# Optimization experiments

Hardware: AMD Instinct MI355X
Metric: run time of the kernel (lower is better)

## Reference

```python
import jax, jax.numpy as jnp
import numpy as np

B, S, D, V = 2, 256, 512, 32000
W_WIN, GAMMA = 20, 2.0
MEM_LEN, NUM_MEM, K_SIM, K_CONT = 16, 256, 8, 4


def _modularity(sim, bnd):
    deg = sim.sum(1)
    tot = deg.sum()
    com = jnp.cumsum(bnd).astype(jnp.int32)
    exp = deg[:, None] * deg[None, :] / (tot + 1e-10)
    mask = (com[:, None] == com[None, :]).astype(sim.dtype)
    return ((sim - exp) * mask).sum() / (tot + 1e-10)


def _conductance(sim, bnd):
    n = sim.shape[0]
    deg = sim.sum(1)
    tot = deg.sum()
    com = jnp.cumsum(bnd).astype(jnp.int32)
    oh = jax.nn.one_hot(com, n + 1, dtype=sim.dtype)  # [N, N+1] fixed class count (empty communities contribute 0)
    vol = oh.T @ deg
    inter = oh.T @ sim @ oh
    inter = inter * (1.0 - jnp.eye(n + 1, dtype=sim.dtype))
    cuts = inter.sum(1)
    minv = jnp.minimum(vol, tot - vol)
    cond = cuts / (minv + 1e-10)
    # torch averages over num_communities = max(com)+1
    return cond.sum() / (com[-1].astype(sim.dtype) + 1.0)


def _forward(query, key, value, attention_mask, target_tokens, brain_w,
             storage_w1, storage_b1, storage_w2, storage_b2, sim_w, sim_b,
             memory_keys, memory_values, memory_lengths, memory_timestamps):
    # --- surprise: per-token NLL of target under brain logits ---
    logits = jnp.einsum('bsd,vd->bsv', query, brain_w)
    logp = jax.nn.log_softmax(logits, axis=-1)
    surprise = -jnp.take_along_axis(logp, target_tokens[..., None], axis=-1)[..., 0]  # [B,S]
    # --- dynamic threshold over sliding windows (unbiased std, as torch) ---
    widx = jnp.arange(S - W_WIN + 1)[:, None] + jnp.arange(W_WIN)[None, :]
    win = surprise[:, widx]  # [B, S-W+1, W]
    thr = win.mean(-1) + GAMMA * jnp.std(win, axis=-1, ddof=1)
    thr = jnp.concatenate([jnp.repeat(thr[:, :1], W_WIN - 1, axis=1), thr], axis=1)
    boundaries = (surprise > thr).astype(query.dtype)  # [B,S]
    # --- refine boundaries via modularity / conductance on token similarity graph ---
    sims = jnp.einsum('bnd,bmd->bnm', query, query)
    curQ = jax.vmap(_modularity)(sims, boundaries)
    curC = jax.vmap(_conductance)(sims, boundaries)
    b_idx = jnp.repeat(jnp.arange(B), S)
    t_idx = jnp.tile(jnp.arange(S), B)

    def cand(b, t):  # evaluate removing boundary at (b,t)
        tb = boundaries[b].at[t].set(0.0)
        return _modularity(sims[b], tb), _conductance(sims[b], tb)

    newQ, newC = jax.vmap(cand)(b_idx, t_idx)
    impr = ((newQ > curQ[b_idx]) | (newC < curC[b_idx])).reshape(B, S)
    refined = jnp.where((boundaries > 0) & impr, 0.0, boundaries)
    # --- event segmentation: labels via cumsum; position-in-event via cummax of segment starts ---
    labels = jnp.cumsum(refined, axis=1).astype(jnp.int32)  # [B,S] in [0,S]
    t_r = jnp.arange(S)
    changed = jnp.concatenate([jnp.ones((B, 1), bool), labels[:, 1:] != labels[:, :-1]], axis=1)
    start = jax.lax.cummax(jnp.where(changed, t_r[None, :], 0), axis=1)
    pos = t_r[None, :] - start  # [B,S] position within event
    bflat = jnp.repeat(jnp.arange(B), S)
    lflat = labels.reshape(-1)
    pflat = pos.reshape(-1)  # tokens with pos >= MEM_LEN are truncated (OOB -> dropped)
    events = jnp.zeros((B, S + 1, MEM_LEN, D), query.dtype)
    events = events.at[bflat, lflat, pflat].add(query.reshape(-1, D), mode='drop')
    counts = jnp.zeros((B, S + 1), jnp.int32).at[bflat, lflat].add(1)
    # --- pack non-empty events into circular memory bank (memory_index = 0, timestamp = 0) ---
    flat_ev = events.reshape(B * (S + 1), MEM_LEN, D)
    flat_ct = counts.reshape(-1)
    nonempty = flat_ct > 0
    rank = jnp.cumsum(nonempty) - 1
    slot = jnp.where(nonempty, rank % NUM_MEM, NUM_MEM)  # OOB slot -> dropped
    mem_keys = memory_keys.at[slot].set(flat_ev[:, 0, :], mode='drop')
    mem_vals = memory_values.at[slot].set(flat_ev, mode='drop')
    mem_lens = memory_lengths.at[slot].set(jnp.minimum(flat_ct, MEM_LEN).astype(memory_lengths.dtype), mode='drop')
    mem_ts = memory_timestamps.at[slot].set(jnp.zeros(slot.shape, memory_timestamps.dtype), mode='drop')
    # --- retrieval: kNN over memory keys with projected mean query ---
    qm = (jnp.einsum('bsd,ed->bse', query, sim_w) + sim_b).mean(1)  # [B,D]
    scores = qm @ mem_keys.T  # [B, NUM_MEM]
    valid = mem_lens > 0
    scores = jnp.where(valid[None, :], scores, -1e9)
    _, top_i = jax.lax.top_k(scores, K_SIM)
    sim_buf = mem_vals[top_i].reshape(B, K_SIM * MEM_LEN, D)
    rec = jnp.where(valid, jnp.arange(NUM_MEM), -1)  # contiguity = most recently written slots
    _, cont_i = jax.lax.top_k(rec, K_CONT)
    cont_buf = jnp.broadcast_to(mem_vals[cont_i].reshape(1, K_CONT * MEM_LEN, D), (B, K_CONT * MEM_LEN, D))
    storage = lambda x: jax.nn.relu(x @ storage_w1.T + storage_b1) @ storage_w2.T + storage_b2
    context = jnp.concatenate([storage(sim_buf), storage(cont_buf), key], axis=1)  # [B, 192+S, D]
    mem_total = (K_SIM + K_CONT) * MEM_LEN
    ext_mask = jnp.concatenate([jnp.ones((B, mem_total), attention_mask.dtype), attention_mask], axis=1)
    return query, context, context, ext_mask


def setup_inputs():
    rng = jax.random.key(0)
    ks = jax.random.split(rng, 10)
    sc = 0.02
    return {
        'query': jax.random.normal(ks[0], (B, S, D), jnp.float32),
        'key': jax.random.normal(ks[1], (B, S, D), jnp.float32),
        'value': jax.random.normal(ks[2], (B, S, D), jnp.float32),
        'attention_mask': jnp.ones((B, S), jnp.float32),
        'target_tokens': jax.random.randint(ks[3], (B, S), 0, V),
        'brain_w': jax.random.normal(ks[4], (V, D), jnp.float32) * sc,
        'storage_w1': jax.random.normal(ks[5], (D, D), jnp.float32) * sc,
        'storage_b1': jnp.zeros((D,), jnp.float32),
        'storage_w2': jax.random.normal(ks[6], (D, D), jnp.float32) * sc,
        'storage_b2': jnp.zeros((D,), jnp.float32),
        'sim_w': jax.random.normal(ks[7], (D, D), jnp.float32) * sc,
        'sim_b': jnp.zeros((D,), jnp.float32),
        'memory_keys': jnp.zeros((NUM_MEM, D), jnp.float32),
        'memory_values': jnp.zeros((NUM_MEM, MEM_LEN, D), jnp.float32),
        'memory_lengths': jnp.zeros((NUM_MEM,), jnp.int32),
        'memory_timestamps': jnp.zeros((NUM_MEM,), jnp.float32),
    }


def reference(query, key, value, attention_mask, target_tokens, brain_w, storage_w1, storage_b1, storage_w2, storage_b2, sim_w, sim_b, memory_keys, memory_values, memory_lengths, memory_timestamps):
    return _forward(query, key, value, attention_mask, target_tokens, brain_w, storage_w1, storage_b1, storage_w2, storage_b2, sim_w, sim_b, memory_keys, memory_values, memory_lengths, memory_timestamps)
```

## Files before the change

kernel.cpp:

```cpp
#include <hip/hip_runtime.h>

constexpr int Bb = 2;
constexpr int Ss = 256;
constexpr int Dd = 512;
constexpr int Vv = 32000;
constexpr int NVB = Vv / 64;
constexpr float GAMMA_C = 2.0f;
constexpr int MEMLEN = 16;
constexpr int NMEM = 256;
constexpr int MTOT = (8 + 4) * MEMLEN;
constexpr int CTXROWS = MTOT + Ss;

constexpr size_t NQ   = (size_t)Bb * Ss * Dd;
constexpr size_t OC1  = NQ;
constexpr size_t NCTX = (size_t)Bb * CTXROWS * Dd;
constexpr size_t OC2  = OC1 + NCTX;
constexpr size_t OMASK = OC2 + NCTX;

constexpr size_t WS_FLOATS_NEEDED = 256000 + 512 + 512 + 131072 + 131584 + 512 +
                                    1024 + 1024 + 512 + 196608 + 196608 + 4096;

__device__ __forceinline__ void gemm64x64_k512(const float* __restrict__ A,
                                               const float* __restrict__ Bm,
                                               float acc[4][4],
                                               float4* __restrict__ Qs4,
                                               float4* __restrict__ Ws4) {
  const int t = threadIdx.x;
  const int tn = t & 15, tm = t >> 4;
  float* __restrict__ Qf = (float*)Qs4;
  float* __restrict__ Wf = (float*)Ws4;
  #pragma unroll 2
  for (int kc = 0; kc < 512; kc += 32) {
    #pragma unroll
    for (int e = 0; e < 2; ++e) {
      const int idx4 = t + 256 * e;
      const int m = idx4 >> 3;
      const int kg = idx4 & 7;
      const float4 qa = *(const float4*)(A + (size_t)m * 512 + kc + kg * 4);
      const float4 wb = *(const float4*)(Bm + (size_t)m * 512 + kc + kg * 4);
      const int fb = ((kg * 4) * 16 + ((m >> 2) ^ kg)) * 4 + (m & 3);
      Qf[fb]       = qa.x; Qf[fb + 64]  = qa.y;
      Qf[fb + 128] = qa.z; Qf[fb + 192] = qa.w;
      Wf[fb]       = wb.x; Wf[fb + 64]  = wb.y;
      Wf[fb + 128] = wb.z; Wf[fb + 192] = wb.w;
    }
    __syncthreads();
    #pragma unroll
    for (int k = 0; k < 32; ++k) {
      const int swz = (k >> 2) & 7;
      const float4 a4 = Qs4[k * 16 + (tm ^ swz)];
      const float4 b4 = Ws4[k * 16 + (tn ^ swz)];
      const float av[4] = {a4.x, a4.y, a4.z, a4.w};
      const float bv[4] = {b4.x, b4.y, b4.z, b4.w};
      #pragma unroll
      for (int i = 0; i < 4; ++i)
        #pragma unroll
        for (int j = 0; j < 4; ++j)
          acc[i][j] += av[i] * bv[j];
    }
    __syncthreads();
  }
}

__global__ __launch_bounds__(256) void k_logits(const float* __restrict__ q,
                                                const float* __restrict__ bw,
                                                float* __restrict__ partial) {
  __shared__ float4 As4[512];
  __shared__ float4 Bs4[1024];
  __shared__ float red[64 * 17];
  const int bv = blockIdx.x;
  const int bm = blockIdx.y;
  const int t = threadIdx.x;
  const int tn = t & 15, tm = t >> 4;
  const float* A  = q  + (size_t)bm * 64 * 512;
  const float* Bm = bw + (size_t)bv * 128 * 512;
  float* Af = (float*)As4;
  float* Bf = (float*)Bs4;
  float acc0[4][4] = {};
  float acc1[4][4] = {};
  #pragma unroll 1
  for (int kc = 0; kc < 512; kc += 32) {
    #pragma unroll
    for (int e = 0; e < 2; ++e) {
      const int idx = t + 256 * e;
      const int m = idx >> 3, kg = idx & 7;
      const float4 v = *(const float4*)(A + (size_t)m * 512 + kc + kg * 4);
      const int fb = ((kg * 4) * 16 + ((m >> 2) ^ kg)) * 4 + (m & 3);
      Af[fb] = v.x; Af[fb + 64] = v.y; Af[fb + 128] = v.z; Af[fb + 192] = v.w;
    }
    #pragma unroll
    for (int e = 0; e < 4; ++e) {
      const int idx = t + 256 * e;
      const int mB = idx >> 3, kg = idx & 7;
      const float4 v = *(const float4*)(Bm + (size_t)mB * 512 + kc + kg * 4);
      const int m4 = mB >> 2;
      const int g = (m4 & 24) | ((m4 & 7) ^ kg);
      const int fb = ((kg * 4) * 32 + g) * 4 + (mB & 3);
      Bf[fb] = v.x; Bf[fb + 128] = v.y; Bf[fb + 256] = v.z; Bf[fb + 384] = v.w;
    }
    __syncthreads();
    #pragma unroll
    for (int k = 0; k < 32; ++k) {
      const int swz = (k >> 2) & 7;
      const float4 a4 = As4[k * 16 + (tm ^ swz)];
      const int g0 = (tn & 8) | ((tn & 7) ^ swz);
      const float4 b0 = Bs4[k * 32 + g0];
      const float4 b1 = Bs4[k * 32 + 16 + g0];
      const float av[4]  = {a4.x, a4.y, a4.z, a4.w};
      const float b0v[4] = {b0.x, b0.y, b0.z, b0.w};
      const float b1v[4] = {b1.x, b1.y, b1.z, b1.w};
      #pragma unroll
      for (int i = 0; i < 4; ++i)
        #pragma unroll
        for (int j = 0; j < 4; ++j) {
          acc0[i][j] += av[i] * b0v[j];
          acc1[i][j] += av[i] * b1v[j];
        }
    }
    __syncthreads();
  }
  #pragma unroll
  for (int i = 0; i < 4; ++i) {
    float s = 0.f;
    #pragma unroll
    for (int j = 0; j < 4; ++j) s += expf(acc0[i][j]);
    red[(tm * 4 + i) * 17 + tn] = s;
  }
  __syncthreads();
  if (t < 64) {
    float s = 0.f;
    #pragma unroll
    for (int j = 0; j < 16; ++j) s += red[t * 17 + j];
    partial[(size_t)(bv * 2) * 512 + bm * 64 + t] = s;
  }
  __syncthreads();
  #pragma unroll
  for (int i = 0; i < 4; ++i) {
    float s = 0.f;
    #pragma unroll
    for (int j = 0; j < 4; ++j) s += expf(acc1[i][j]);
    red[(tm * 4 + i) * 17 + tn] = s;
  }
  __syncthreads();
  if (t < 64) {
    float s = 0.f;
    #pragma unroll
    for (int j = 0; j < 16; ++j) s += red[t * 17 + j];
    partial[(size_t)(bv * 2 + 1) * 512 + bm * 64 + t] = s;
  }
}

constexpr int MISC_SIMS = 32;
constexpr int MISC_QBAR = MISC_SIMS + 4;
constexpr int MISC_LSE  = MISC_QBAR + 16;
constexpr int MISC_NBLK = MISC_LSE + 2052;

__global__ __launch_bounds__(256) void k_misc(const float* __restrict__ q,
                                              const float* __restrict__ key,
                                              const float* __restrict__ amask,
                                              const float* __restrict__ partial,
                                              float* __restrict__ sims,
                                              float* __restrict__ qbar,
                                              double* __restrict__ pc,
                                              float* __restrict__ out) {
  __shared__ float4 sh4[1024];
  const int bx = blockIdx.x, t = threadIdx.x;
  if (bx < MISC_SIMS) {
    int b = bx >> 4, rem = bx & 15;
    int m0 = (rem >> 2) * 64, n0 = (rem & 3) * 64;
    float acc[4][4] = {};
    const float* qb = q + (size_t)b * Ss * Dd;
    gemm64x64_k512(qb + (size_t)m0 * 512, qb + (size_t)n0 * 512, acc, sh4, sh4 + 512);
    int tn = t & 15, tm = t >> 4;
    float* outp = sims + (size_t)b * Ss * Ss;
    #pragma unroll
    for (int i = 0; i < 4; ++i) {
      float4 v = make_float4(acc[i][0], acc[i][1], acc[i][2], acc[i][3]);
      *(float4*)&outp[(size_t)(m0 + tm * 4 + i) * 256 + n0 + tn * 4] = v;
    }
  } else if (bx < MISC_QBAR) {
    int id = (bx - MISC_SIMS) * 256 + t;
    int b = id >> 9, d = id & 511;
    float s = 0.f;
    for (int ss2 = 0; ss2 < 256; ++ss2) s += q[((size_t)(b * 256 + ss2)) * 512 + d];
    qbar[id] = s * (1.0f / 256.0f);
  } else if (bx < MISC_LSE) {
    int idx = bx - MISC_QBAR;
    int c = idx >> 1, rb = idx & 1;
    int r = rb * 256 + t;
    int j0 = c * 63, j1 = (j0 + 63 < NVB) ? j0 + 63 : NVB;
    double s = 0.0;
    for (int j = j0; j < j1; ++j) s += (double)partial[(size_t)j * 512 + r];
    pc[c * 512 + r] = s;
  } else {
    int id = (bx - MISC_LSE) * 256 + t;
    if (id < 262144) { out[id] = q[id]; return; }
    if (id < 524288) {
      int id2 = id - 262144;
      int b = id2 >> 17;
      int s = (id2 >> 9) & 255;
      int d = id2 & 511;
      float v = key[id2];
      size_t p = OC1 + ((size_t)(b * 448 + 192 + s)) * 512 + d;
      out[p] = v;
      out[p + NCTX] = v;
      return;
    }
    if (id < 525184) {
      int j = id - 524288;
      int b = j / 448, c = j - b * 448;
      out[OMASK + j] = (c < 192) ? 1.0f : amask[b * 256 + (c - 192)];
    }
  }
}

__global__ __launch_bounds__(256) void k_sur(const float* __restrict__ q,
                                             const float* __restrict__ bw,
                                             const int* __restrict__ tgt,
                                             const double* __restrict__ pc,
                                             float* __restrict__ sur) {
  int wid = blockIdx.x * 4 + (threadIdx.x >> 6);
  int lane = threadIdx.x & 63;
  int tg = tgt[wid];
  const float* qp = q + (size_t)wid * 512;
  const float* wp = bw + (size_t)tg * 512;
  float a = 0.f;
  #pragma unroll
  for (int j = 0; j < 8; ++j) a += qp[lane + 64 * j] * wp[lane + 64 * j];
  #pragma unroll
  for (int off = 32; off; off >>= 1) a += __shfl_xor(a, off);
  if (lane == 0) {
    double s = 0.0;
    #pragma unroll
    for (int c = 0; c < 8; ++c) s += pc[c * 512 + wid];
    float lsef = (float)log(s);
    sur[wid] = lsef - a;
  }
}

__global__ __launch_bounds__(256) void k_bound(const float* __restrict__ sur,
                                               int* __restrict__ bnd) {
  __shared__ float ss[256];
  __shared__ float thrw[237];
  int b = blockIdx.x, t = threadIdx.x;
  ss[t] = sur[b * 256 + t];
  __syncthreads();
  if (t < 237) {
    float mn = 0.f;
    #pragma unroll
    for (int e = 0; e < 20; ++e) mn += ss[t + e];
    mn *= (1.0f / 20.0f);
    float v = 0.f;
    #pragma unroll
    for (int e = 0; e < 20; ++e) { float d = ss[t + e] - mn; v += d * d; }
    thrw[t] = mn + GAMMA_C * sqrtf(v * (1.0f / 19.0f));
  }
  __syncthreads();
  float th = (t <= 18) ? thrw[0] : thrw[t - 19];
  bnd[b * 256 + t] = (ss[t] > th) ? 1 : 0;
}

__global__ __launch_bounds__(256) void k_rowpref(const float* __restrict__ sims,
                                                 float* __restrict__ R,
                                                 float* __restrict__ deg) {
  int wid = blockIdx.x * 4 + (threadIdx.x >> 6);
  int lane = threadIdx.x & 63;
  int b = wid >> 8, i = wid & 255;
  const float* row = sims + (size_t)b * 65536 + (size_t)i * 256;
  float4 v = *(const float4*)&row[lane * 4];
  float c0 = v.x, c1 = c0 + v.y, c2 = c1 + v.z, c3 = c2 + v.w;
  float ls = c3;
  float sc = ls;
  for (int off = 1; off < 64; off <<= 1) {
    float u = __shfl_up(sc, off);
    if (lane >= off) sc += u;
  }
  float ex = sc - ls;
  float* Rr = R + (size_t)b * (256 * 257) + (size_t)i * 257;
  Rr[lane * 4 + 1] = ex + c0;
  Rr[lane * 4 + 2] = ex + c1;
  Rr[lane * 4 + 3] = ex + c2;
  Rr[lane * 4 + 4] = ex + c3;
  if (lane == 0) Rr[0] = 0.f;
  if (lane == 63) deg[b * 256 + i] = ex + c3;
}

__global__ __launch_bounds__(256) void k_refine(const int* __restrict__ bnd,
                                                const float* __restrict__ R,
                                                const float* __restrict__ deg,
                                                int* __restrict__ nseg,
                                                int* __restrict__ segstart_o,
                                                int* __restrict__ segcnt_o) {
  __shared__ int sb[256], lab[256];
  __shared__ int segst[258];
  __shared__ float Dc[257], Sc[257], Cr[257];
  __shared__ float degsh[256];
  __shared__ float Stm[256], Ctm[256];
  __shared__ float sh[6];
  int b = blockIdx.x, t = threadIdx.x;
  sb[t] = bnd[b * 256 + t];
  degsh[t] = deg[b * 256 + t];
  for (int c = t; c < 258; c += 256) segst[c] = -1;
  __syncthreads();
  int a = 0;
  for (int i = 0; i <= t; ++i) a += sb[i];
  lab[t] = a;
  __syncthreads();
  if (t == 0 || lab[t - 1] != lab[t]) segst[lab[t]] = t;
  __syncthreads();
  int nb = lab[255];
  const float* Rb = R + (size_t)b * (256 * 257);
  {
    int c = lab[t];
    int a1 = segst[c];
    int e1 = (c == nb) ? 255 : (segst[c + 1] - 1);
    const float* Rrow = Rb + (size_t)t * 257;
    Stm[t] = Rrow[e1 + 1] - Rrow[a1];
    float cv = 0.f;
    if (c < nb) {
      int a2 = segst[c + 1];
      int e2 = (c + 1 == nb) ? 255 : (segst[c + 2] - 1);
      cv = Rrow[e2 + 1] - Rrow[a2];
    }
    Ctm[t] = cv;
  }
  __syncthreads();
  for (int c = t; c <= nb; c += 256) {
    float Dv = 0.f, Sv = 0.f, Cv = 0.f;
    int a1 = segst[c];
    if (a1 >= 0) {
      int e1 = (c == nb) ? 255 : (segst[c + 1] - 1);
      for (int i = a1; i <= e1; ++i) { Dv += degsh[i]; Sv += Stm[i]; Cv += Ctm[i]; }
    }
    Dc[c] = Dv; Sc[c] = Sv; Cr[c] = Cv;
  }
  __syncthreads();
  if (t == 0) {
    float tot = 0.f;
    for (int i = 0; i < 256; ++i) tot += degsh[i];
    float tote = tot + 1e-10f;
    float Qun = 0.f, Cs = 0.f;
    for (int c = 0; c <= nb; ++c) {
      Qun += Sc[c] - Dc[c] * Dc[c] / tote;
      Cs  += (Dc[c] - Sc[c]) / (fminf(Dc[c], tot - Dc[c]) + 1e-10f);
    }
    sh[0] = tot; sh[1] = tote; sh[2] = Qun; sh[3] = Cs;
    sh[4] = Qun / tote; sh[5] = Cs / (float)(nb + 1);
  }
  __syncthreads();
  int r = sb[t];
  if (r == 1) {
    float tot = sh[0], tote = sh[1], Qun = sh[2], Cs = sh[3], curQ = sh[4], curC = sh[5];
    int c2 = lab[t], c1 = c2 - 1;
    if (segst[c1] < 0) {
      float newC0 = Cs / (float)nb;
      if (newC0 < curC) r = 0;
    } else {
      float D1 = Dc[c1], S1 = Sc[c1], D2 = Dc[c2], S2 = Sc[c2];
      float Dm = D1 + D2, Sm = S1 + S2 + 2.0f * Cr[c1];
      float tq1 = S1 - D1 * D1 / tote;
      float tq2 = S2 - D2 * D2 / tote;
      float tqm = Sm - Dm * Dm / tote;
      float newQ = (Qun - tq1 - tq2 + tqm) / tote;
      float tc1 = (D1 - S1) / (fminf(D1, tot - D1) + 1e-10f);
      float tc2 = (D2 - S2) / (fminf(D2, tot - D2) + 1e-10f);
      float tcm = (Dm - Sm) / (fminf(Dm, tot - Dm) + 1e-10f);
      float newC = (Cs - tc1 - tc2 + tcm) / (float)nb;
      if (newQ > curQ || newC < curC) r = 0;
    }
  }
  __syncthreads();
  sb[t] = r;
  __syncthreads();
  if (t == 0) {
    int ns = 0, st = 0;
    for (int i = 1; i <= 256; ++i) {
      if (i == 256 || sb[i] == 1) {
        segstart_o[b * 257 + ns] = st;
        segcnt_o[b * 257 + ns] = i - st;
        ns++;
        st = i;
      }
    }
    nseg[b] = ns;
  }
}

__global__ __launch_bounds__(256) void k_slots(const int* __restrict__ nseg,
                                               const int* __restrict__ segstart_i,
                                               const int* __restrict__ segcnt_i,
                                               const int* __restrict__ meml_in,
                                               int* __restrict__ slot_b,
                                               int* __restrict__ slot_start,
                                               int* __restrict__ slot_cnt,
                                               int* __restrict__ cont) {
  __shared__ unsigned char validsh[256];
  __shared__ int ns01[2];
  int t = threadIdx.x;
  if (t < 2) ns01[t] = nseg[t];
  __syncthreads();
  int ns0 = ns01[0], total = ns0 + ns01[1];
  int rank = -1;
  for (int r = t; r < total; r += 256) rank = r;
  int bb = 0, st = 0, ct = 0;
  if (rank >= 0) {
    bb = (rank >= ns0) ? 1 : 0;
    int s = rank - bb * ns0;
    st = segstart_i[bb * 257 + s];
    ct = segcnt_i[bb * 257 + s];
  }
  slot_b[t] = bb; slot_start[t] = st; slot_cnt[t] = ct;
  validsh[t] = (ct > 0 || meml_in[t] > 0) ? 1 : 0;
  __syncthreads();
  if (t == 0) {
    int k = 0;
    for (int n = 255; n >= 0 && k < 4; --n) if (validsh[n]) cont[k++] = n;
    for (int n = 0; n < 256 && k < 4; ++n) if (!validsh[n]) cont[k++] = n;
  }
}

__global__ __launch_bounds__(256) void k_qm(const float* __restrict__ qbar,
                                            const float* __restrict__ simw,
                                            const float* __restrict__ simb,
                                            float* __restrict__ qm) {
  int wid = blockIdx.x * 4 + (threadIdx.x >> 6);
  int lane = threadIdx.x & 63;
  int b = wid >> 9, e = wid & 511;
  float a = 0.f;
  #pragma unroll
  for (int j = 0; j < 8; ++j)
    a += qbar[b * 512 + lane + 64 * j] * simw[(size_t)e * 512 + lane + 64 * j];
  #pragma unroll
  for (int off = 32; off; off >>= 1) a += __shfl_xor(a, off);
  if (lane == 0) qm[b * 512 + e] = a + simb[e];
}

__global__ __launch_bounds__(256) void k_scores(const float* __restrict__ q,
                                                const float* __restrict__ memk,
                                                const int* __restrict__ meml,
                                                const int* __restrict__ slot_b,
                                                const int* __restrict__ slot_start,
                                                const int* __restrict__ slot_cnt,
                                                const float* __restrict__ qm,
                                                float* __restrict__ scores) {
  int wid = blockIdx.x * 4 + (threadIdx.x >> 6);
  int lane = threadIdx.x & 63;
  int b = wid >> 8, n = wid & 255;
  const float* kp = nullptr;
  if (slot_cnt[n] > 0) kp = q + ((size_t)(slot_b[n] * 256 + slot_start[n])) * 512;
  else if (meml[n] > 0) kp = memk + (size_t)n * 512;
  float a = 0.f;
  if (kp) {
    #pragma unroll
    for (int j = 0; j < 8; ++j) a += qm[b * 512 + lane + 64 * j] * kp[lane + 64 * j];
    #pragma unroll
    for (int off = 32; off; off >>= 1) a += __shfl_xor(a, off);
  }
  if (lane == 0) scores[b * 256 + n] = kp ? a : -1000000000.0f;
}

__global__ __launch_bounds__(64) void k_topk(const float* __restrict__ scores,
                                             int* __restrict__ topi) {
  int b = blockIdx.x, lane = threadIdx.x;
  float v[4];
  #pragma unroll
  for (int j = 0; j < 4; ++j) v[j] = scores[b * 256 + lane * 4 + j];
  int chosen = 0;
  for (int k = 0; k < 8; ++k) {
    float best = -3.4e38f; int bi = 0x7fffffff;
    #pragma unroll
    for (int j = 0; j < 4; ++j) {
      if (!(chosen & (1 << j))) {
        float s = v[j]; int n = lane * 4 + j;
        if (s > best || (s == best && n < bi)) { best = s; bi = n; }
      }
    }
    #pragma unroll
    for (int off = 32; off; off >>= 1) {
      float ob = __shfl_xor(best, off);
      int oi = __shfl_xor(bi, off);
      if (ob > best || (ob == best && oi < bi)) { best = ob; bi = oi; }
    }
    if ((bi >> 2) == lane) chosen |= 1 << (bi & 3);
    if (lane == 0) topi[b * 8 + k] = bi;
  }
}

__global__ __launch_bounds__(256) void k_gather(const float* __restrict__ q,
                                                const float* __restrict__ memv,
                                                const int* __restrict__ topi,
                                                const int* __restrict__ cont,
                                                const int* __restrict__ slot_b,
                                                const int* __restrict__ slot_start,
                                                const int* __restrict__ slot_cnt,
                                                float* __restrict__ xg) {
  int id = blockIdx.x * 256 + threadIdx.x;
  int d = id & 511;
  int rb = id >> 9;
  int b = rb / 192;
  int r = rb - b * 192;
  int p = r & 15;
  int slot = (r < 128) ? topi[b * 8 + (r >> 4)] : cont[(r - 128) >> 4];
  float val;
  int cnt = slot_cnt[slot];
  if (cnt > 0) {
    int ml = cnt < 16 ? cnt : 16;
    val = (p < ml) ? q[((size_t)(slot_b[slot] * 256 + slot_start[slot] + p)) * 512 + d] : 0.f;
  } else {
    val = memv[((size_t)slot * 16 + p) * 512 + d];
  }
  xg[id] = val;
}

__global__ __launch_bounds__(256) void k_mlp1(const float* __restrict__ xg,
                                              const float* __restrict__ w1,
                                              const float* __restrict__ b1,
                                              float* __restrict__ h) {
  __shared__ float4 Qs4[512];
  __shared__ float4 Ws4[512];
  int n0 = blockIdx.x * 64, m0 = blockIdx.y * 64;
  float acc[4][4] = {};
  gemm64x64_k512(xg + (size_t)m0 * 512, w1 + (size_t)n0 * 512, acc, Qs4, Ws4);
  int t = threadIdx.x, tn = t & 15, tm = t >> 4;
  #pragma unroll
  for (int i = 0; i < 4; ++i) {
    int m = m0 + tm * 4 + i;
    #pragma unroll
    for (int j = 0; j < 4; ++j) {
      int n = n0 + tn * 4 + j;
      h[(size_t)m * 512 + n] = fmaxf(acc[i][j] + b1[n], 0.f);
    }
  }
}

__global__ __launch_bounds__(256) void k_mlp2(const float* __restrict__ h,
                                              const float* __restrict__ w2,
                                              const float* __restrict__ b2,
                                              float* __restrict__ out) {
  __shared__ float4 Qs4[512];
  __shared__ float4 Ws4[512];
  int n0 = blockIdx.x * 64, m0 = blockIdx.y * 64;
  float acc[4][4] = {};
  gemm64x64_k512(h + (size_t)m0 * 512, w2 + (size_t)n0 * 512, acc, Qs4, Ws4);
  int t = threadIdx.x, tn = t & 15, tm = t >> 4;
  #pragma unroll
  for (int i = 0; i < 4; ++i) {
    int m = m0 + tm * 4 + i;
    int b = (m >= 192) ? 1 : 0;
    int rr = m - b * 192;
    int n = n0 + tn * 4;
    float4 v = make_float4(acc[i][0] + b2[n], acc[i][1] + b2[n + 1],
                           acc[i][2] + b2[n + 2], acc[i][3] + b2[n + 3]);
    size_t base = OC1 + ((size_t)(b * 448 + rr)) * 512 + n;
    *(float4*)&out[base] = v;
    *(float4*)&out[base + NCTX] = v;
  }
}

extern "C" void kernel_launch(void* const* d_in, const int* in_sizes, int n_in,
                              void* d_out, int out_size, void* d_ws, size_t ws_size,
                              hipStream_t stream) {
  if (ws_size < WS_FLOATS_NEEDED * sizeof(float)) return;

  const float* q     = (const float*)d_in[0];
  const float* key   = (const float*)d_in[1];
  const float* amask = (const float*)d_in[3];
  const int*   tgt   = (const int*)d_in[4];
  const float* bw    = (const float*)d_in[5];
  const float* w1    = (const float*)d_in[6];
  const float* b1    = (const float*)d_in[7];
  const float* w2    = (const float*)d_in[8];
  const float* b2    = (const float*)d_in[9];
  const float* simw  = (const float*)d_in[10];
  const float* simb  = (const float*)d_in[11];
  const float* memk  = (const float*)d_in[12];
  const float* memv  = (const float*)d_in[13];
  const int*   meml  = (const int*)d_in[14];
  float* out = (float*)d_out;

  float* w = (float*)d_ws;
  float* p_partial = w;
  float* p_lse    = p_partial + 256000;
  float* p_sur    = p_lse + 512;
  float* p_sims   = p_sur + 512;
  float* p_R      = p_sims + 131072;
  float* p_deg    = p_R + 131584;
  float* p_qbar   = p_deg + 512;
  float* p_qm     = p_qbar + 1024;
  float* p_scores = p_qm + 1024;
  float* p_xg     = p_scores + 512;
  float* p_h      = p_xg + 196608;
  double* p_pc    = (double*)p_h;
  int* ip         = (int*)(p_h + 196608);
  int* ip_bnd     = ip;
  int* ip_nseg    = ip + 512;
  int* ip_segst   = ip + 514;
  int* ip_segcnt  = ip + 1028;
  int* ip_slotb   = ip + 1542;
  int* ip_slotst  = ip + 1798;
  int* ip_slotcnt = ip + 2054;
  int* ip_topi    = ip + 2310;
  int* ip_cont    = ip + 2326;

  k_logits<<<dim3(250, 8), 256, 0, stream>>>(q, bw, p_partial);
  k_misc<<<MISC_NBLK, 256, 0, stream>>>(q, key, amask, p_partial,
                                        p_sims, p_qbar, p_pc, out);
  k_sur<<<128, 256, 0, stream>>>(q, bw, tgt, p_pc, p_sur);
  k_bound<<<2, 256, 0, stream>>>(p_sur, ip_bnd);
  k_rowpref<<<128, 256, 0, stream>>>(p_sims, p_R, p_deg);
  k_refine<<<2, 256, 0, stream>>>(ip_bnd, p_R, p_deg, ip_nseg, ip_segst, ip_segcnt);
  k_slots<<<1, 256, 0, stream>>>(ip_nseg, ip_segst, ip_segcnt, meml,
                                 ip_slotb, ip_slotst, ip_slotcnt, ip_cont);
  k_qm<<<256, 256, 0, stream>>>(p_qbar, simw, simb, p_qm);
  k_scores<<<128, 256, 0, stream>>>(q, memk, meml, ip_slotb, ip_slotst, ip_slotcnt,
                                    p_qm, p_scores);
  k_topk<<<2, 64, 0, stream>>>(p_scores, ip_topi);
  k_gather<<<768, 256, 0, stream>>>(q, memv, ip_topi, ip_cont,
                                    ip_slotb, ip_slotst, ip_slotcnt, p_xg);
  k_mlp1<<<dim3(8, 6), 256, 0, stream>>>(p_xg, w1, b1, p_h);
  k_mlp2<<<dim3(8, 6), 256, 0, stream>>>(p_h, w2, b2, out);
}
```

Before: 485.0 us.

## Fuse post-logits kernels into one cooperative grid kernel and enlarge logits tile

The thirteen small kernels that ran after the logits GEMM are merged into a single cooperative kernel of 128 blocks, with grid-wide syncs between phases. This removes per-launch overhead and the idle gaps between tiny dependent kernels. Separately, the logits GEMM tile grows from 64 to 128 query rows per block, so each block computes four 4x4 accumulators and halves the grid to 250x4, giving more reuse of the loaded vocabulary weights. In exchange, the heavy copy phase now runs on only 76 blocks, many grid syncs leave most blocks idle, and register pressure in the logits kernel rises.

```diff
diff --git a/kernel.cpp b/kernel.cpp
--- a/kernel.cpp
+++ b/kernel.cpp
@@ -1,4 +1,7 @@
 #include <hip/hip_runtime.h>
+#include <hip/hip_cooperative_groups.h>
+
+namespace cg = cooperative_groups;
 
 constexpr int Bb = 2;
 constexpr int Ss = 256;
@@ -65,27 +68,30 @@
 __global__ __launch_bounds__(256) void k_logits(const float* __restrict__ q,
                                                 const float* __restrict__ bw,
                                                 float* __restrict__ partial) {
-  __shared__ float4 As4[512];
+  __shared__ float4 As4[1024];
   __shared__ float4 Bs4[1024];
   __shared__ float red[64 * 17];
   const int bv = blockIdx.x;
   const int bm = blockIdx.y;
   const int t = threadIdx.x;
   const int tn = t & 15, tm = t >> 4;
-  const float* A  = q  + (size_t)bm * 64 * 512;
+  const float* A  = q  + (size_t)bm * 128 * 512;
   const float* Bm = bw + (size_t)bv * 128 * 512;
   float* Af = (float*)As4;
   float* Bf = (float*)Bs4;
-  float acc0[4][4] = {};
-  float acc1[4][4] = {};
+  float acc00[4][4] = {};
+  float acc01[4][4] = {};
+  float acc10[4][4] = {};
+  float acc11[4][4] = {};
   #pragma unroll 1
   for (int kc = 0; kc < 512; kc += 32) {
     #pragma unroll
-    for (int e = 0; e < 2; ++e) {
+    for (int e = 0; e < 4; ++e) {
       const int idx = t + 256 * e;
-      const int m = idx >> 3, kg = idx & 7;
-      const float4 v = *(const float4*)(A + (size_t)m * 512 + kc + kg * 4);
-      const int fb = ((kg * 4) * 16 + ((m >> 2) ^ kg)) * 4 + (m & 3);
+      const int mf = idx >> 3, kg = idx & 7;
+      const float4 v = *(const float4*)(A + (size_t)mf * 512 + kc + kg * 4);
+      const int h = mf >> 6, m = mf & 63;
+      const int fb = h * 2048 + ((kg * 4) * 16 + ((m >> 2) ^ kg)) * 4 + (m & 3);
       Af[fb] = v.x; Af[fb + 64] = v.y; Af[fb + 128] = v.z; Af[fb + 192] = v.w;
     }
     #pragma unroll
@@ -102,458 +108,451 @@
     #pragma unroll
     for (int k = 0; k < 32; ++k) {
       const int swz = (k >> 2) & 7;
-      const float4 a4 = As4[k * 16 + (tm ^ swz)];
+      const float4 alo = As4[k * 16 + (tm ^ swz)];
+      const float4 ahi = As4[512 + k * 16 + (tm ^ swz)];
       const int g0 = (tn & 8) | ((tn & 7) ^ swz);
       const float4 b0 = Bs4[k * 32 + g0];
       const float4 b1 = Bs4[k * 32 + 16 + g0];
-      const float av[4]  = {a4.x, a4.y, a4.z, a4.w};
+      const float al[4] = {alo.x, alo.y, alo.z, alo.w};
+      const float ah[4] = {ahi.x, ahi.y, ahi.z, ahi.w};
       const float b0v[4] = {b0.x, b0.y, b0.z, b0.w};
       const float b1v[4] = {b1.x, b1.y, b1.z, b1.w};
       #pragma unroll
       for (int i = 0; i < 4; ++i)
         #pragma unroll
         for (int j = 0; j < 4; ++j) {
-          acc0[i][j] += av[i] * b0v[j];
-          acc1[i][j] += av[i] * b1v[j];
+          acc00[i][j] += al[i] * b0v[j];
+          acc01[i][j] += al[i] * b1v[j];
+          acc10[i][j] += ah[i] * b0v[j];
+          acc11[i][j] += ah[i] * b1v[j];
         }
     }
     __syncthreads();
   }
   #pragma unroll
-  for (int i = 0; i < 4; ++i) {
-    float s = 0.f;
-    #pragma unroll
-    for (int j = 0; j < 4; ++j) s += expf(acc0[i][j]);
-    red[(tm * 4 + i) * 17 + tn] = s;
-  }
-  __syncthreads();
-  if (t < 64) {
-    float s = 0.f;
-    #pragma unroll
-    for (int j = 0; j < 16; ++j) s += red[t * 17 + j];
-    partial[(size_t)(bv * 2) * 512 + bm * 64 + t] = s;
-  }
-  __syncthreads();
-  #pragma unroll
-  for (int i = 0; i < 4; ++i) {
-    float s = 0.f;
-    #pragma unroll
-    for (int j = 0; j < 4; ++j) s += expf(acc1[i][j]);
-    red[(tm * 4 + i) * 17 + tn] = s;
-  }
-  __syncthreads();
-  if (t < 64) {
-    float s = 0.f;
-    #pragma unroll
-    for (int j = 0; j < 16; ++j) s += red[t * 17 + j];
-    partial[(size_t)(bv * 2 + 1) * 512 + bm * 64 + t] = s;
+  for (int h = 0; h < 2; ++h) {
+    #pragma unroll
+    for (int band = 0; band < 2; ++band) {
+      #pragma unroll
+      for (int i = 0; i < 4; ++i) {
+        float s = 0.f;
+        #pragma unroll
+        for (int j = 0; j < 4; ++j) {
+          float v = (h == 0) ? ((band == 0) ? acc00[i][j] : acc01[i][j])
+                             : ((band == 0) ? acc10[i][j] : acc11[i][j]);
+          s += expf(v);
+        }
+        red[(tm * 4 + i) * 17 + tn] = s;
+      }
+      __syncthreads();
+      if (t < 64) {
+        float s = 0.f;
+        #pragma unroll
+        for (int j = 0; j < 16; ++j) s += red[t * 17 + j];
+        partial[(size_t)(bv * 2 + band) * 512 + bm * 128 + h * 64 + t] = s;
+      }
+      __syncthreads();
+    }
   }
 }
 
-constexpr int MISC_SIMS = 32;
-constexpr int MISC_QBAR = MISC_SIMS + 4;
-constexpr int MISC_LSE  = MISC_QBAR + 16;
-constexpr int MISC_NBLK = MISC_LSE + 2052;
-
-__global__ __launch_bounds__(256) void k_misc(const float* __restrict__ q,
-                                              const float* __restrict__ key,
-                                              const float* __restrict__ amask,
-                                              const float* __restrict__ partial,
-                                              float* __restrict__ sims,
-                                              float* __restrict__ qbar,
-                                              double* __restrict__ pc,
-                                              float* __restrict__ out) {
-  __shared__ float4 sh4[1024];
-  const int bx = blockIdx.x, t = threadIdx.x;
-  if (bx < MISC_SIMS) {
-    int b = bx >> 4, rem = bx & 15;
+struct CoopParams {
+  const float* q;
+  const float* key;
+  const float* amask;
+  const float* bw;
+  const int*   tgt;
+  const float* partial;
+  const float* simw;
+  const float* simb;
+  const int*   meml;
+  const float* memk;
+  const float* memv;
+  const float* w1;
+  const float* b1;
+  const float* w2;
+  const float* b2;
+  float* sims;
+  float* qbar;
+  double* pc;
+  float* R;
+  float* deg;
+  float* sur;
+  int* bnd;
+  int* nseg;
+  int* segst;
+  int* segcnt;
+  int* slotb;
+  int* slotst;
+  int* slotcnt;
+  int* cont;
+  int* topi;
+  float* qm;
+  float* scores;
+  float* xg;
+  float* h;
+  float* out;
+};
+
+__global__ __launch_bounds__(256) void k_coop(CoopParams P) {
+  cg::grid_group gg = cg::this_grid();
+  __shared__ __align__(16) char smem[16640];
+  const int b = blockIdx.x, t = threadIdx.x;
+  const int wv = t >> 6, lane = t & 63;
+
+  if (b < 32) {
+    float4* Qs4 = (float4*)smem;
+    float4* Ws4 = Qs4 + 512;
+    int bb = b >> 4, rem = b & 15;
     int m0 = (rem >> 2) * 64, n0 = (rem & 3) * 64;
     float acc[4][4] = {};
-    const float* qb = q + (size_t)b * Ss * Dd;
-    gemm64x64_k512(qb + (size_t)m0 * 512, qb + (size_t)n0 * 512, acc, sh4, sh4 + 512);
+    const float* qb = P.q + (size_t)bb * Ss * Dd;
+    gemm64x64_k512(qb + (size_t)m0 * 512, qb + (size_t)n0 * 512, acc, Qs4, Ws4);
     int tn = t & 15, tm = t >> 4;
-    float* outp = sims + (size_t)b * Ss * Ss;
+    float* outp = P.sims + (size_t)bb * Ss * Ss;
     #pragma unroll
     for (int i = 0; i < 4; ++i) {
       float4 v = make_float4(acc[i][0], acc[i][1], acc[i][2], acc[i][3]);
       *(float4*)&outp[(size_t)(m0 + tm * 4 + i) * 256 + n0 + tn * 4] = v;
     }
-  } else if (bx < MISC_QBAR) {
-    int id = (bx - MISC_SIMS) * 256 + t;
-    int b = id >> 9, d = id & 511;
+  } else if (b < 36) {
+    int id = (b - 32) * 256 + t;
+    int bb = id >> 9, d = id & 511;
     float s = 0.f;
-    for (int ss2 = 0; ss2 < 256; ++ss2) s += q[((size_t)(b * 256 + ss2)) * 512 + d];
-    qbar[id] = s * (1.0f / 256.0f);
-  } else if (bx < MISC_LSE) {
-    int idx = bx - MISC_QBAR;
+    for (int ss2 = 0; ss2 < 256; ++ss2) s += P.q[((size_t)(bb * 256 + ss2)) * 512 + d];
+    P.qbar[id] = s * (1.0f / 256.0f);
+  } else if (b < 52) {
+    int idx = b - 36;
     int c = idx >> 1, rb = idx & 1;
     int r = rb * 256 + t;
     int j0 = c * 63, j1 = (j0 + 63 < NVB) ? j0 + 63 : NVB;
     double s = 0.0;
-    for (int j = j0; j < j1; ++j) s += (double)partial[(size_t)j * 512 + r];
-    pc[c * 512 + r] = s;
+    for (int j = j0; j < j1; ++j) s += (double)P.partial[(size_t)j * 512 + r];
+    P.pc[c * 512 + r] = s;
   } else {
-    int id = (bx - MISC_LSE) * 256 + t;
-    if (id < 262144) { out[id] = q[id]; return; }
-    if (id < 524288) {
-      int id2 = id - 262144;
-      int b = id2 >> 17;
-      int s = (id2 >> 9) & 255;
-      int d = id2 & 511;
-      float v = key[id2];
-      size_t p = OC1 + ((size_t)(b * 448 + 192 + s)) * 512 + d;
-      out[p] = v;
-      out[p + NCTX] = v;
-      return;
-    }
-    if (id < 525184) {
-      int j = id - 524288;
-      int b = j / 448, c = j - b * 448;
-      out[OMASK + j] = (c < 192) ? 1.0f : amask[b * 256 + (c - 192)];
-    }
-  }
-}
-
-__global__ __launch_bounds__(256) void k_sur(const float* __restrict__ q,
-                                             const float* __restrict__ bw,
-                                             const int* __restrict__ tgt,
-                                             const double* __restrict__ pc,
-                                             float* __restrict__ sur) {
-  int wid = blockIdx.x * 4 + (threadIdx.x >> 6);
-  int lane = threadIdx.x & 63;
-  int tg = tgt[wid];
-  const float* qp = q + (size_t)wid * 512;
-  const float* wp = bw + (size_t)tg * 512;
-  float a = 0.f;
-  #pragma unroll
-  for (int j = 0; j < 8; ++j) a += qp[lane + 64 * j] * wp[lane + 64 * j];
-  #pragma unroll
-  for (int off = 32; off; off >>= 1) a += __shfl_xor(a, off);
-  if (lane == 0) {
-    double s = 0.0;
-    #pragma unroll
-    for (int c = 0; c < 8; ++c) s += pc[c * 512 + wid];
-    float lsef = (float)log(s);
-    sur[wid] = lsef - a;
-  }
-}
-
-__global__ __launch_bounds__(256) void k_bound(const float* __restrict__ sur,
-                                               int* __restrict__ bnd) {
-  __shared__ float ss[256];
-  __shared__ float thrw[237];
-  int b = blockIdx.x, t = threadIdx.x;
-  ss[t] = sur[b * 256 + t];
-  __syncthreads();
-  if (t < 237) {
-    float mn = 0.f;
-    #pragma unroll
-    for (int e = 0; e < 20; ++e) mn += ss[t + e];
-    mn *= (1.0f / 20.0f);
-    float v = 0.f;
-    #pragma unroll
-    for (int e = 0; e < 20; ++e) { float d = ss[t + e] - mn; v += d * d; }
-    thrw[t] = mn + GAMMA_C * sqrtf(v * (1.0f / 19.0f));
-  }
-  __syncthreads();
-  float th = (t <= 18) ? thrw[0] : thrw[t - 19];
-  bnd[b * 256 + t] = (ss[t] > th) ? 1 : 0;
-}
-
-__global__ __launch_bounds__(256) void k_rowpref(const float* __restrict__ sims,
-                                                 float* __restrict__ R,
-                                                 float* __restrict__ deg) {
-  int wid = blockIdx.x * 4 + (threadIdx.x >> 6);
-  int lane = threadIdx.x & 63;
-  int b = wid >> 8, i = wid & 255;
-  const float* row = sims + (size_t)b * 65536 + (size_t)i * 256;
-  float4 v = *(const float4*)&row[lane * 4];
-  float c0 = v.x, c1 = c0 + v.y, c2 = c1 + v.z, c3 = c2 + v.w;
-  float ls = c3;
-  float sc = ls;
-  for (int off = 1; off < 64; off <<= 1) {
-    float u = __shfl_up(sc, off);
-    if (lane >= off) sc += u;
-  }
-  float ex = sc - ls;
-  float* Rr = R + (size_t)b * (256 * 257) + (size_t)i * 257;
-  Rr[lane * 4 + 1] = ex + c0;
-  Rr[lane * 4 + 2] = ex + c1;
-  Rr[lane * 4 + 3] = ex + c2;
-  Rr[lane * 4 + 4] = ex + c3;
-  if (lane == 0) Rr[0] = 0.f;
-  if (lane == 63) deg[b * 256 + i] = ex + c3;
-}
-
-__global__ __launch_bounds__(256) void k_refine(const int* __restrict__ bnd,
-                                                const float* __restrict__ R,
-                                                const float* __restrict__ deg,
-                                                int* __restrict__ nseg,
-                                                int* __restrict__ segstart_o,
-                                                int* __restrict__ segcnt_o) {
-  __shared__ int sb[256], lab[256];
-  __shared__ int segst[258];
-  __shared__ float Dc[257], Sc[257], Cr[257];
-  __shared__ float degsh[256];
-  __shared__ float Stm[256], Ctm[256];
-  __shared__ float sh[6];
-  int b = blockIdx.x, t = threadIdx.x;
-  sb[t] = bnd[b * 256 + t];
-  degsh[t] = deg[b * 256 + t];
-  for (int c = t; c < 258; c += 256) segst[c] = -1;
-  __syncthreads();
-  int a = 0;
-  for (int i = 0; i <= t; ++i) a += sb[i];
-  lab[t] = a;
-  __syncthreads();
-  if (t == 0 || lab[t - 1] != lab[t]) segst[lab[t]] = t;
-  __syncthreads();
-  int nb = lab[255];
-  const float* Rb = R + (size_t)b * (256 * 257);
+    for (int ci = b - 52; ci < 2052; ci += 76) {
+      int id = ci * 256 + t;
+      if (id < 262144) {
+        P.out[id] = P.q[id];
+      } else if (id < 524288) {
+        int id2 = id - 262144;
+        int bb = id2 >> 17;
+        int s = (id2 >> 9) & 255;
+        int d = id2 & 511;
+        float v = P.key[id2];
+        size_t p = OC1 + ((size_t)(bb * 448 + 192 + s)) * 512 + d;
+        P.out[p] = v;
+        P.out[p + NCTX] = v;
+      } else if (id < 525184) {
+        int j = id - 524288;
+        int bb = j / 448, c = j - bb * 448;
+        P.out[OMASK + j] = (c < 192) ? 1.0f : P.amask[bb * 256 + (c - 192)];
+      }
+    }
+  }
+  gg.sync();
+
   {
-    int c = lab[t];
-    int a1 = segst[c];
-    int e1 = (c == nb) ? 255 : (segst[c + 1] - 1);
-    const float* Rrow = Rb + (size_t)t * 257;
-    Stm[t] = Rrow[e1 + 1] - Rrow[a1];
-    float cv = 0.f;
-    if (c < nb) {
-      int a2 = segst[c + 1];
-      int e2 = (c + 1 == nb) ? 255 : (segst[c + 2] - 1);
-      cv = Rrow[e2 + 1] - Rrow[a2];
-    }
-    Ctm[t] = cv;
-  }
-  __syncthreads();
-  for (int c = t; c <= nb; c += 256) {
-    float Dv = 0.f, Sv = 0.f, Cv = 0.f;
-    int a1 = segst[c];
-    if (a1 >= 0) {
+    int wid = b * 4 + wv;
+    {
+      int tg = P.tgt[wid];
+      const float* qp = P.q + (size_t)wid * 512;
+      const float* wp = P.bw + (size_t)tg * 512;
+      float a = 0.f;
+      #pragma unroll
+      for (int j = 0; j < 8; ++j) a += qp[lane + 64 * j] * wp[lane + 64 * j];
+      #pragma unroll
+      for (int off = 32; off; off >>= 1) a += __shfl_xor(a, off);
+      if (lane == 0) {
+        double s = 0.0;
+        #pragma unroll
+        for (int c = 0; c < 8; ++c) s += P.pc[c * 512 + wid];
+        P.sur[wid] = (float)log(s) - a;
+      }
+    }
+    {
+      int bb = wid >> 8, i = wid & 255;
+      const float* row = P.sims + (size_t)bb * 65536 + (size_t)i * 256;
+      float4 v = *(const float4*)&row[lane * 4];
+      float c0 = v.x, c1 = c0 + v.y, c2 = c1 + v.z, c3 = c2 + v.w;
+      float ls = c3;
+      float sc = ls;
+      for (int off = 1; off < 64; off <<= 1) {
+        float u = __shfl_up(sc, off);
+        if (lane >= off) sc += u;
+      }
+      float ex = sc - ls;
+      float* Rr = P.R + (size_t)bb * (256 * 257) + (size_t)i * 257;
+      Rr[lane * 4 + 1] = ex + c0;
+      Rr[lane * 4 + 2] = ex + c1;
+      Rr[lane * 4 + 3] = ex + c2;
+      Rr[lane * 4 + 4] = ex + c3;
+      if (lane == 0) Rr[0] = 0.f;
+      if (lane == 63) P.deg[bb * 256 + i] = ex + c3;
+    }
+    #pragma unroll
+    for (int half = 0; half < 2; ++half) {
+      int wid2 = half * 512 + wid;
+      int bb = wid2 >> 9, e = wid2 & 511;
+      float a = 0.f;
+      #pragma unroll
+      for (int j = 0; j < 8; ++j)
+        a += P.qbar[bb * 512 + lane + 64 * j] * P.simw[(size_t)e * 512 + lane + 64 * j];
+      #pragma unroll
+      for (int off = 32; off; off >>= 1) a += __shfl_xor(a, off);
+      if (lane == 0) P.qm[bb * 512 + e] = a + P.simb[e];
+    }
+  }
+  gg.sync();
+
+  if (b < 2) {
+    float* ss = (float*)smem;
+    float* thrw = ss + 256;
+    ss[t] = P.sur[b * 256 + t];
+    __syncthreads();
+    if (t < 237) {
+      float mn = 0.f;
+      #pragma unroll
+      for (int e = 0; e < 20; ++e) mn += ss[t + e];
+      mn *= (1.0f / 20.0f);
+      float v = 0.f;
+      #pragma unroll
+      for (int e = 0; e < 20; ++e) { float d = ss[t + e] - mn; v += d * d; }
+      thrw[t] = mn + GAMMA_C * sqrtf(v * (1.0f / 19.0f));
+    }
+    __syncthreads();
+    float th = (t <= 18) ? thrw[0] : thrw[t - 19];
+    P.bnd[b * 256 + t] = (ss[t] > th) ? 1 : 0;
+  }
+  gg.sync();
+
+  if (b < 2) {
+    int* sb    = (int*)smem;
+    int* lab   = sb + 256;
+    int* segst = lab + 256;
+    float* Dc    = (float*)(segst + 258);
+    float* Sc    = Dc + 257;
+    float* Cr    = Sc + 257;
+    float* degsh = Cr + 257;
+    float* Stm   = degsh + 256;
+    float* Ctm   = Stm + 256;
+    float* sh    = Ctm + 256;
+    sb[t] = P.bnd[b * 256 + t];
+    degsh[t] = P.deg[b * 256 + t];
+    for (int c = t; c < 258; c += 256) segst[c] = -1;
+    __syncthreads();
+    int a = 0;
+    for (int i = 0; i <= t; ++i) a += sb[i];
+    lab[t] = a;
+    __syncthreads();
+    if (t == 0 || lab[t - 1] != lab[t]) segst[lab[t]] = t;
+    __syncthreads();
+    int nb = lab[255];
+    const float* Rb = P.R + (size_t)b * (256 * 257);
+    {
+      int c = lab[t];
+      int a1 = segst[c];
       int e1 = (c == nb) ? 255 : (segst[c + 1] - 1);
-      for (int i = a1; i <= e1; ++i) { Dv += degsh[i]; Sv += Stm[i]; Cv += Ctm[i]; }
-    }
-    Dc[c] = Dv; Sc[c] = Sv; Cr[c] = Cv;
-  }
-  __syncthreads();
-  if (t == 0) {
-    float tot = 0.f;
-    for (int i = 0; i < 256; ++i) tot += degsh[i];
-    float tote = tot + 1e-10f;
-    float Qun = 0.f, Cs = 0.f;
-    for (int c = 0; c <= nb; ++c) {
-      Qun += Sc[c] - Dc[c] * Dc[c] / tote;
-      Cs  += (Dc[c] - Sc[c]) / (fminf(Dc[c], tot - Dc[c]) + 1e-10f);
-    }
-    sh[0] = tot; sh[1] = tote; sh[2] = Qun; sh[3] = Cs;
-    sh[4] = Qun / tote; sh[5] = Cs / (float)(nb + 1);
-  }
-  __syncthreads();
-  int r = sb[t];
-  if (r == 1) {
-    float tot = sh[0], tote = sh[1], Qun = sh[2], Cs = sh[3], curQ = sh[4], curC = sh[5];
-    int c2 = lab[t], c1 = c2 - 1;
-    if (segst[c1] < 0) {
-      float newC0 = Cs / (float)nb;
-      if (newC0 < curC) r = 0;
+      const float* Rrow = Rb + (size_t)t * 257;
+      Stm[t] = Rrow[e1 + 1] - Rrow[a1];
+      float cv = 0.f;
+      if (c < nb) {
+        int a2 = segst[c + 1];
+        int e2 = (c + 1 == nb) ? 255 : (segst[c + 2] - 1);
+        cv = Rrow[e2 + 1] - Rrow[a2];
+      }
+      Ctm[t] = cv;
+    }
+    __syncthreads();
+    for (int c = t; c <= nb; c += 256) {
+      float Dv = 0.f, Sv = 0.f, Cv = 0.f;
+      int a1 = segst[c];
+      if (a1 >= 0) {
+        int e1 = (c == nb) ? 255 : (segst[c + 1] - 1);
+        for (int i = a1; i <= e1; ++i) { Dv += degsh[i]; Sv += Stm[i]; Cv += Ctm[i]; }
+      }
+      Dc[c] = Dv; Sc[c] = Sv; Cr[c] = Cv;
+    }
+    __syncthreads();
+    if (t == 0) {
+      float tot = 0.f;
+      for (int i = 0; i < 256; ++i) tot += degsh[i];
+      float tote = tot + 1e-10f;
+      float Qun = 0.f, Cs = 0.f;
+      for (int c = 0; c <= nb; ++c) {
+        Qun += Sc[c] - Dc[c] * Dc[c] / tote;
+        Cs  += (Dc[c] - Sc[c]) / (fminf(Dc[c], tot - Dc[c]) + 1e-10f);
+      }
+      sh[0] = tot; sh[1] = tote; sh[2] = Qun; sh[3] = Cs;
+      sh[4] = Qun / tote; sh[5] = Cs / (float)(nb + 1);
+    }
+    __syncthreads();
+    int r = sb[t];
+    if (r == 1) {
+      float tot = sh[0], tote = sh[1], Qun = sh[2], Cs = sh[3], curQ = sh[4], curC = sh[5];
+      int c2 = lab[t], c1 = c2 - 1;
+      if (segst[c1] < 0) {
+        float newC0 = Cs / (float)nb;
+        if (newC0 < curC) r = 0;
+      } else {
+        float D1 = Dc[c1], S1 = Sc[c1], D2 = Dc[c2], S2 = Sc[c2];
+        float Dm = D1 + D2, Sm = S1 + S2 + 2.0f * Cr[c1];
+        float tq1 = S1 - D1 * D1 / tote;
+        float tq2 = S2 - D2 * D2 / tote;
+        float tqm = Sm - Dm * Dm / tote;
+        float newQ = (Qun - tq1 - tq2 + tqm) / tote;
+        float tc1 = (D1 - S1) / (fminf(D1, tot - D1) + 1e-10f);
+        float tc2 = (D2 - S2) / (fminf(D2, tot - D2) + 1e-10f);
+        float tcm = (Dm - Sm) / (fminf(Dm, tot - Dm) + 1e-10f);
+        float newC = (Cs - tc1 - tc2 + tcm) / (float)nb;
+        if (newQ > curQ || newC < curC) r = 0;
+      }
+    }
+    __syncthreads();
+    sb[t] = r;
+    __syncthreads();
+    if (t == 0) {
+      int ns = 0, st = 0;
+      for (int i = 1; i <= 256; ++i) {
+        if (i == 256 || sb[i] == 1) {
+          P.segst[b * 257 + ns] = st;
+          P.segcnt[b * 257 + ns] = i - st;
+          ns++;
+          st = i;
+        }
+      }
+      P.nseg[b] = ns;
+    }
+  }
+  gg.sync();
+
+  if (b == 0) {
+    unsigned char* validsh = (unsigned char*)smem;
+    int* ns01 = (int*)(smem + 256);
+    if (t < 2) ns01[t] = P.nseg[t];
+    __syncthreads();
+    int ns0 = ns01[0], total = ns0 + ns01[1];
+    int rank = -1;
+    for (int r = t; r < total; r += 256) rank = r;
+    int bb = 0, st = 0, ct = 0;
+    if (rank >= 0) {
+      bb = (rank >= ns0) ? 1 : 0;
+      int s = rank - bb * ns0;
+      st = P.segst[bb * 257 + s];
+      ct = P.segcnt[bb * 257 + s];
+    }
+    P.slotb[t] = bb; P.slotst[t] = st; P.slotcnt[t] = ct;
+    validsh[t] = (ct > 0 || P.meml[t] > 0) ? 1 : 0;
+    __syncthreads();
+    if (t == 0) {
+      int k = 0;
+      for (int n = 255; n >= 0 && k < 4; --n) if (validsh[n]) P.cont[k++] = n;
+      for (int n = 0; n < 256 && k < 4; ++n) if (!validsh[n]) P.cont[k++] = n;
+    }
+  }
+  gg.sync();
+
+  {
+    int wid = b * 4 + wv;
+    int bb = wid >> 8, n = wid & 255;
+    const float* kp = nullptr;
+    if (P.slotcnt[n] > 0) kp = P.q + ((size_t)(P.slotb[n] * 256 + P.slotst[n])) * 512;
+    else if (P.meml[n] > 0) kp = P.memk + (size_t)n * 512;
+    float a = 0.f;
+    if (kp) {
+      #pragma unroll
+      for (int j = 0; j < 8; ++j) a += P.qm[bb * 512 + lane + 64 * j] * kp[lane + 64 * j];
+      #pragma unroll
+      for (int off = 32; off; off >>= 1) a += __shfl_xor(a, off);
+    }
+    if (lane == 0) P.scores[bb * 256 + n] = kp ? a : -1000000000.0f;
+  }
+  gg.sync();
+
+  if (b < 2 && t < 64) {
+    float v[4];
+    #pragma unroll
+    for (int j = 0; j < 4; ++j) v[j] = P.scores[b * 256 + t * 4 + j];
+    int chosen = 0;
+    for (int k = 0; k < 8; ++k) {
+      float best = -3.4e38f; int bi = 0x7fffffff;
+      #pragma unroll
+      for (int j = 0; j < 4; ++j) {
+        if (!(chosen & (1 << j))) {
+          float s = v[j]; int n = t * 4 + j;
+          if (s > best || (s == best && n < bi)) { best = s; bi = n; }
+        }
+      }
+      #pragma unroll
+      for (int off = 32; off; off >>= 1) {
+        float ob = __shfl_xor(best, off);
+        int oi = __shfl_xor(bi, off);
+        if (ob > best || (ob == best && oi < bi)) { best = ob; bi = oi; }
+      }
+      if ((bi >> 2) == t) chosen |= 1 << (bi & 3);
+      if (t == 0) P.topi[b * 8 + k] = bi;
+    }
+  }
+  gg.sync();
+
+  for (int gi = b; gi < 768; gi += 128) {
+    int id = gi * 256 + t;
+    int d = id & 511;
+    int rb = id >> 9;
+    int bb = rb / 192;
+    int r = rb - bb * 192;
+    int p = r & 15;
+    int slot = (r < 128) ? P.topi[bb * 8 + (r >> 4)] : P.cont[(r - 128) >> 4];
+    float val;
+    int cnt = P.slotcnt[slot];
+    if (cnt > 0) {
+      int ml = cnt < 16 ? cnt : 16;
+      val = (p < ml) ? P.q[((size_t)(P.slotb[slot] * 256 + P.slotst[slot] + p)) * 512 + d] : 0.f;
     } else {
-      float D1 = Dc[c1], S1 = Sc[c1], D2 = Dc[c2], S2 = Sc[c2];
-      float Dm = D1 + D2, Sm = S1 + S2 + 2.0f * Cr[c1];
-      float tq1 = S1 - D1 * D1 / tote;
-      float tq2 = S2 - D2 * D2 / tote;
-      float tqm = Sm - Dm * Dm / tote;
-      float newQ = (Qun - tq1 - tq2 + tqm) / tote;
-      float tc1 = (D1 - S1) / (fminf(D1, tot - D1) + 1e-10f);
-      float tc2 = (D2 - S2) / (fminf(D2, tot - D2) + 1e-10f);
-      float tcm = (Dm - Sm) / (fminf(Dm, tot - Dm) + 1e-10f);
-      float newC = (Cs - tc1 - tc2 + tcm) / (float)nb;
-      if (newQ > curQ || newC < curC) r = 0;
-    }
-  }
-  __syncthreads();
-  sb[t] = r;
-  __syncthreads();
-  if (t == 0) {
-    int ns = 0, st = 0;
-    for (int i = 1; i <= 256; ++i) {
-      if (i == 256 || sb[i] == 1) {
-        segstart_o[b * 257 + ns] = st;
-        segcnt_o[b * 257 + ns] = i - st;
-        ns++;
-        st = i;
-      }
-    }
-    nseg[b] = ns;
-  }
-}
-
-__global__ __launch_bounds__(256) void k_slots(const int* __restrict__ nseg,
-                                               const int* __restrict__ segstart_i,
-                                               const int* __restrict__ segcnt_i,
-                                               const int* __restrict__ meml_in,
-                                               int* __restrict__ slot_b,
-                                               int* __restrict__ slot_start,
-                                               int* __restrict__ slot_cnt,
-                                               int* __restrict__ cont) {
-  __shared__ unsigned char validsh[256];
-  __shared__ int ns01[2];
-  int t = threadIdx.x;
-  if (t < 2) ns01[t] = nseg[t];
-  __syncthreads();
-  int ns0 = ns01[0], total = ns0 + ns01[1];
-  int rank = -1;
-  for (int r = t; r < total; r += 256) rank = r;
-  int bb = 0, st = 0, ct = 0;
-  if (rank >= 0) {
-    bb = (rank >= ns0) ? 1 : 0;
-    int s = rank - bb * ns0;
-    st = segstart_i[bb * 257 + s];
-    ct = segcnt_i[bb * 257 + s];
-  }
-  slot_b[t] = bb; slot_start[t] = st; slot_cnt[t] = ct;
-  validsh[t] = (ct > 0 || meml_in[t] > 0) ? 1 : 0;
-  __syncthreads();
-  if (t == 0) {
-    int k = 0;
-    for (int n = 255; n >= 0 && k < 4; --n) if (validsh[n]) cont[k++] = n;
-    for (int n = 0; n < 256 && k < 4; ++n) if (!validsh[n]) cont[k++] = n;
-  }
-}
-
-__global__ __launch_bounds__(256) void k_qm(const float* __restrict__ qbar,
-                                            const float* __restrict__ simw,
-                                            const float* __restrict__ simb,
-                                            float* __restrict__ qm) {
-  int wid = blockIdx.x * 4 + (threadIdx.x >> 6);
-  int lane = threadIdx.x & 63;
-  int b = wid >> 9, e = wid & 511;
-  float a = 0.f;
-  #pragma unroll
-  for (int j = 0; j < 8; ++j)
-    a += qbar[b * 512 + lane + 64 * j] * simw[(size_t)e * 512 + lane + 64 * j];
-  #pragma unroll
-  for (int off = 32; off; off >>= 1) a += __shfl_xor(a, off);
-  if (lane == 0) qm[b * 512 + e] = a + simb[e];
-}
-
-__global__ __launch_bounds__(256) void k_scores(const float* __restrict__ q,
-                                                const float* __restrict__ memk,
-                                                const int* __restrict__ meml,
-                                                const int* __restrict__ slot_b,
-                                                const int* __restrict__ slot_start,
-                                                const int* __restrict__ slot_cnt,
-                                                const float* __restrict__ qm,
-                                                float* __restrict__ scores) {
-  int wid = blockIdx.x * 4 + (threadIdx.x >> 6);
-  int lane = threadIdx.x & 63;
-  int b = wid >> 8, n = wid & 255;
-  const float* kp = nullptr;
-  if (slot_cnt[n] > 0) kp = q + ((size_t)(slot_b[n] * 256 + slot_start[n])) * 512;
-  else if (meml[n] > 0) kp = memk + (size_t)n * 512;
-  float a = 0.f;
-  if (kp) {
-    #pragma unroll
-    for (int j = 0; j < 8; ++j) a += qm[b * 512 + lane + 64 * j] * kp[lane + 64 * j];
-    #pragma unroll
-    for (int off = 32; off; off >>= 1) a += __shfl_xor(a, off);
-  }
-  if (lane == 0) scores[b * 256 + n] = kp ? a : -1000000000.0f;
-}
-
-__global__ __launch_bounds__(64) void k_topk(const float* __restrict__ scores,
-                                             int* __restrict__ topi) {
-  int b = blockIdx.x, lane = threadIdx.x;
-  float v[4];
-  #pragma unroll
-  for (int j = 0; j < 4; ++j) v[j] = scores[b * 256 + lane * 4 + j];
-  int chosen = 0;
-  for (int k = 0; k < 8; ++k) {
-    float best = -3.4e38f; int bi = 0x7fffffff;
-    #pragma unroll
-    for (int j = 0; j < 4; ++j) {
-      if (!(chosen & (1 << j))) {
-        float s = v[j]; int n = lane * 4 + j;
-        if (s > best || (s == best && n < bi)) { best = s; bi = n; }
-      }
-    }
-    #pragma unroll
-    for (int off = 32; off; off >>= 1) {
-      float ob = __shfl_xor(best, off);
-      int oi = __shfl_xor(bi, off);
-      if (ob > best || (ob == best && oi < bi)) { best = ob; bi = oi; }
-    }
-    if ((bi >> 2) == lane) chosen |= 1 << (bi & 3);
-    if (lane == 0) topi[b * 8 + k] = bi;
-  }
-}
-
-__global__ __launch_bounds__(256) void k_gather(const float* __restrict__ q,
-                                                const float* __restrict__ memv,
-                                                const int* __restrict__ topi,
-                                                const int* __restrict__ cont,
-                                                const int* __restrict__ slot_b,
-                                                const int* __restrict__ slot_start,
-                                                const int* __restrict__ slot_cnt,
-                                                float* __restrict__ xg) {
-  int id = blockIdx.x * 256 + threadIdx.x;
-  int d = id & 511;
-  int rb = id >> 9;
-  int b = rb / 192;
-  int r = rb - b * 192;
-  int p = r & 15;
-  int slot = (r < 128) ? topi[b * 8 + (r >> 4)] : cont[(r - 128) >> 4];
-  float val;
-  int cnt = slot_cnt[slot];
-  if (cnt > 0) {
-    int ml = cnt < 16 ? cnt : 16;
-    val = (p < ml) ? q[((size_t)(slot_b[slot] * 256 + slot_start[slot] + p)) * 512 + d] : 0.f;
-  } else {
-    val = memv[((size_t)slot * 16 + p) * 512 + d];
-  }
-  xg[id] = val;
-}
-
-__global__ __launch_bounds__(256) void k_mlp1(const float* __restrict__ xg,
-                                              const float* __restrict__ w1,
-                                              const float* __restrict__ b1,
-                                              float* __restrict__ h) {
-  __shared__ float4 Qs4[512];
-  __shared__ float4 Ws4[512];
-  int n0 = blockIdx.x * 64, m0 = blockIdx.y * 64;
-  float acc[4][4] = {};
-  gemm64x64_k512(xg + (size_t)m0 * 512, w1 + (size_t)n0 * 512, acc, Qs4, Ws4);
-  int t = threadIdx.x, tn = t & 15, tm = t >> 4;
-  #pragma unroll
-  for (int i = 0; i < 4; ++i) {
-    int m = m0 + tm * 4 + i;
-    #pragma unroll
-    for (int j = 0; j < 4; ++j) {
-      int n = n0 + tn * 4 + j;
-      h[(size_t)m * 512 + n] = fmaxf(acc[i][j] + b1[n], 0.f);
-    }
-  }
-}
-
-__global__ __launch_bounds__(256) void k_mlp2(const float* __restrict__ h,
-                                              const float* __restrict__ w2,
-                                              const float* __restrict__ b2,
-                                              float* __restrict__ out) {
-  __shared__ float4 Qs4[512];
-  __shared__ float4 Ws4[512];
-  int n0 = blockIdx.x * 64, m0 = blockIdx.y * 64;
-  float acc[4][4] = {};
-  gemm64x64_k512(h + (size_t)m0 * 512, w2 + (size_t)n0 * 512, acc, Qs4, Ws4);
-  int t = threadIdx.x, tn = t & 15, tm = t >> 4;
-  #pragma unroll
-  for (int i = 0; i < 4; ++i) {
-    int m = m0 + tm * 4 + i;
-    int b = (m >= 192) ? 1 : 0;
-    int rr = m - b * 192;
-    int n = n0 + tn * 4;
-    float4 v = make_float4(acc[i][0] + b2[n], acc[i][1] + b2[n + 1],
-                           acc[i][2] + b2[n + 2], acc[i][3] + b2[n + 3]);
-    size_t base = OC1 + ((size_t)(b * 448 + rr)) * 512 + n;
-    *(float4*)&out[base] = v;
-    *(float4*)&out[base + NCTX] = v;
+      val = P.memv[((size_t)slot * 16 + p) * 512 + d];
+    }
+    P.xg[id] = val;
+  }
+  gg.sync();
+
+  if (b < 48) {
+    float4* Qs4 = (float4*)smem;
+    float4* Ws4 = Qs4 + 512;
+    int n0 = (b & 7) * 64, m0 = (b >> 3) * 64;
+    float acc[4][4] = {};
+    gemm64x64_k512(P.xg + (size_t)m0 * 512, P.w1 + (size_t)n0 * 512, acc, Qs4, Ws4);
+    int tn = t & 15, tm = t >> 4;
+    #pragma unroll
+    for (int i = 0; i < 4; ++i) {
+      int m = m0 + tm * 4 + i;
+      #pragma unroll
+      for (int j = 0; j < 4; ++j) {
+        int n = n0 + tn * 4 + j;
+        P.h[(size_t)m * 512 + n] = fmaxf(acc[i][j] + P.b1[n], 0.f);
+      }
+    }
+  }
+  gg.sync();
+
+  if (b < 48) {
+    float4* Qs4 = (float4*)smem;
+    float4* Ws4 = Qs4 + 512;
+    int n0 = (b & 7) * 64, m0 = (b >> 3) * 64;
+    float acc[4][4] = {};
+    gemm64x64_k512(P.h + (size_t)m0 * 512, P.w2 + (size_t)n0 * 512, acc, Qs4, Ws4);
+    int tn = t & 15, tm = t >> 4;
+    #pragma unroll
+    for (int i = 0; i < 4; ++i) {
+      int m = m0 + tm * 4 + i;
+      int bb = (m >= 192) ? 1 : 0;
+      int rr = m - bb * 192;
+      int n = n0 + tn * 4;
+      float4 v = make_float4(acc[i][0] + P.b2[n], acc[i][1] + P.b2[n + 1],
+                             acc[i][2] + P.b2[n + 2], acc[i][3] + P.b2[n + 3]);
+      size_t base = OC1 + ((size_t)(bb * 448 + rr)) * 512 + n;
+      *(float4*)&P.out[base] = v;
+      *(float4*)&P.out[base + NCTX] = v;
+    }
   }
 }
 
@@ -602,21 +601,20 @@
   int* ip_topi    = ip + 2310;
   int* ip_cont    = ip + 2326;
 
-  k_logits<<<dim3(250, 8), 256, 0, stream>>>(q, bw, p_partial);
-  k_misc<<<MISC_NBLK, 256, 0, stream>>>(q, key, amask, p_partial,
-                                        p_sims, p_qbar, p_pc, out);
-  k_sur<<<128, 256, 0, stream>>>(q, bw, tgt, p_pc, p_sur);
-  k_bound<<<2, 256, 0, stream>>>(p_sur, ip_bnd);
-  k_rowpref<<<128, 256, 0, stream>>>(p_sims, p_R, p_deg);
-  k_refine<<<2, 256, 0, stream>>>(ip_bnd, p_R, p_deg, ip_nseg, ip_segst, ip_segcnt);
-  k_slots<<<1, 256, 0, stream>>>(ip_nseg, ip_segst, ip_segcnt, meml,
-                                 ip_slotb, ip_slotst, ip_slotcnt, ip_cont);
-  k_qm<<<256, 256, 0, stream>>>(p_qbar, simw, simb, p_qm);
-  k_scores<<<128, 256, 0, stream>>>(q, memk, meml, ip_slotb, ip_slotst, ip_slotcnt,
-                                    p_qm, p_scores);
-  k_topk<<<2, 64, 0, stream>>>(p_scores, ip_topi);
-  k_gather<<<768, 256, 0, stream>>>(q, memv, ip_topi, ip_cont,
-                                    ip_slotb, ip_slotst, ip_slotcnt, p_xg);
-  k_mlp1<<<dim3(8, 6), 256, 0, stream>>>(p_xg, w1, b1, p_h);
-  k_mlp2<<<dim3(8, 6), 256, 0, stream>>>(p_h, w2, b2, out);
+  k_logits<<<dim3(250, 4), 256, 0, stream>>>(q, bw, p_partial);
+
+  CoopParams P;
+  P.q = q; P.key = key; P.amask = amask; P.bw = bw; P.tgt = tgt;
+  P.partial = p_partial; P.simw = simw; P.simb = simb;
+  P.meml = meml; P.memk = memk; P.memv = memv;
+  P.w1 = w1; P.b1 = b1; P.w2 = w2; P.b2 = b2;
+  P.sims = p_sims; P.qbar = p_qbar; P.pc = p_pc;
+  P.R = p_R; P.deg = p_deg; P.sur = p_sur;
+  P.bnd = ip_bnd; P.nseg = ip_nseg; P.segst = ip_segst; P.segcnt = ip_segcnt;
+  P.slotb = ip_slotb; P.slotst = ip_slotst; P.slotcnt = ip_slotcnt;
+  P.cont = ip_cont; P.topi = ip_topi;
+  P.qm = p_qm; P.scores = p_scores; P.xg = p_xg; P.h = p_h; P.out = out;
+
+  void* kargs[] = {(void*)&P};
+  hipLaunchCooperativeKernel((const void*)k_coop, dim3(128), dim3(256), kargs, 0, stream);
 }
```

New measurement: 613.5 us. 1.26x slower.
